# Kernel optimization log

Hardware: AMD Instinct MI355X
Metric: run time of the kernel (lower is better)

## Reference

```python
import jax, jax.numpy as jnp
import numpy as np

HIDDEN = 1024
NUM_HEADS = 8
HEAD_DIM = HIDDEN // NUM_HEADS
ROPE_BASE = 10000.0
RMS_EPS = 1e-6


def _rotate_half(x):
    # interleaved rotate: (x0,x1,x2,x3,...) -> (-x1,x0,-x3,x2,...)
    x1 = x[..., ::2]
    x2 = x[..., 1::2]
    return jnp.stack([-x2, x1], axis=-1).reshape(x.shape)


def _rope_cos_sin(seq_len, rotary_dim, dtype):
    inv_freq = 1.0 / (ROPE_BASE ** (jnp.arange(0, rotary_dim, 2, dtype=jnp.float32) / rotary_dim))
    pos = jnp.arange(seq_len, dtype=jnp.float32)
    freqs = pos[:, None] * inv_freq[None, :]            # [S, rd/2]
    cos = jnp.repeat(jnp.cos(freqs), 2, axis=-1)        # [S, rd]
    sin = jnp.repeat(jnp.sin(freqs), 2, axis=-1)
    return cos.astype(dtype)[None, None], sin.astype(dtype)[None, None]


def setup_inputs() -> dict:
    key = jax.random.key(0)
    k = jax.random.split(key, 8)
    B, S, H = 2, 2048, HIDDEN
    hidden_states = jax.random.normal(k[0], (B, S, H), dtype=jnp.float32)
    attention_mask = jax.random.randint(k[1], (B, S, S), 0, 2) > 0
    rel_ts_bias = jax.random.normal(k[2], (B, S, S), dtype=jnp.float32)
    s1 = 1.0 / np.sqrt(H)
    W_qkvu = jax.random.normal(k[3], (H, H * 6), dtype=jnp.float32) * s1
    W_out = jax.random.normal(k[4], (H * 3, H), dtype=jnp.float32) * (1.0 / np.sqrt(H * 3))
    b_out = jnp.zeros((H,), dtype=jnp.float32)
    rms_weight = jnp.ones((H,), dtype=jnp.float32)
    return {"hidden_states": hidden_states, "attention_mask": attention_mask,
            "rel_ts_bias": rel_ts_bias, "W_qkvu": W_qkvu, "W_out": W_out,
            "b_out": b_out, "rms_weight": rms_weight}


def reference(hidden_states, attention_mask, rel_ts_bias, W_qkvu, W_out, b_out, rms_weight):
    B, S, H = hidden_states.shape
    nh, hd = NUM_HEADS, HEAD_DIM
    fused = jax.nn.silu(hidden_states @ W_qkvu)          # [B,S,6H]
    gated = fused[..., :3 * H]                            # [B,S,3H]
    v = fused[..., 3 * H:4 * H].reshape(B, S, nh, hd).transpose(0, 2, 1, 3)
    q = fused[..., 4 * H:5 * H].reshape(B, S, nh, hd).transpose(0, 2, 1, 3)
    kk = fused[..., 5 * H:].reshape(B, S, nh, hd).transpose(0, 2, 1, 3)

    cos, sin = _rope_cos_sin(S, hd, hidden_states.dtype)  # rotary_dim == head_dim
    q_rope = q * cos + _rotate_half(q) * sin
    k_rope = kk * cos + _rotate_half(kk) * sin

    inv_s = 1.0 / max(S, 1)
    qk = jax.nn.relu(jnp.einsum('bhnd,bhmd->bhnm', q, kk)) * inv_s
    qk_rope = jax.nn.relu(jnp.einsum('bhnd,bhmd->bhnm', q_rope, k_rope)) * inv_s

    mask = attention_mask[:, None]                        # [B,1,S,S]
    qk = jnp.where(mask, qk, 0.0)
    qk_rope = jnp.where(mask, qk_rope, 0.0)
    ts_bias = jnp.where(attention_mask, rel_ts_bias, 0.0)

    ts_out = jnp.einsum('bnm,bhmd->bnhd', ts_bias, v)
    rope_out = jnp.einsum('bhnm,bhmd->bnhd', qk_rope, v)
    plain_out = jnp.einsum('bhnm,bhmd->bnhd', qk, v)

    combined = jnp.concatenate([rope_out, ts_out, plain_out], axis=-1).reshape(B, S, 3 * H)
    out = (combined * gated) @ W_out + b_out
    y = out + hidden_states
    rms = jax.lax.rsqrt(jnp.mean(y * y, axis=-1, keepdims=True) + RMS_EPS)
    return y * rms * rms_weight
```

## Files before the change

kernel.cpp:

```cpp
#include <hip/hip_runtime.h>
#include <math.h>

static constexpr int Bz = 2;
static constexpr int Sq = 2048;
static constexpr int Hh = 1024;
static constexpr int NH = 8;
static constexpr int HD = 128;
static constexpr int H3 = 3072;
static constexpr int H6 = 6144;

typedef unsigned short ushort_t;
typedef float f32x4v __attribute__((ext_vector_type(4)));
typedef short s16x8 __attribute__((ext_vector_type(8)));

static constexpr size_t FUSED_OFF = 0;
static constexpr size_t A2_OFF    = 12582912;
static constexpr size_t HB_OFF    = 18874368;
static constexpr size_t WQT_OFF   = 20971520;
static constexpr size_t WOT_OFF   = 24117248;
static constexpr size_t QR_OFF    = 25690112;
static constexpr size_t KR_OFF    = 27787264;
static constexpr size_t VT_OFF    = 29884416;
static constexpr size_t TAB_OFF   = 31981568;
static constexpr size_t FLAG_OFF  = 32243712;
static constexpr size_t TSB_OFF   = 32243716;
static constexpr size_t MBITS_OFF = 36438020;

__device__ __forceinline__ float silu_(float x) { return x / (1.0f + expf(-x)); }
__device__ __forceinline__ ushort_t f2bf(float x) {
  unsigned int u = __float_as_uint(x);
  u += 0x7fffu + ((u >> 16) & 1u);
  return (ushort_t)(u >> 16);
}
__device__ __forceinline__ float bf2f(ushort_t u) {
  return __uint_as_float(((unsigned int)u) << 16);
}
__device__ __forceinline__ void g2l16(const ushort_t* g, ushort_t* l) {
  __builtin_amdgcn_global_load_lds(
      (const __attribute__((address_space(1))) unsigned int*)g,
      (__attribute__((address_space(3))) unsigned int*)l, 16, 0, 0);
}

__global__ __launch_bounds__(256) void hstu_cvt_all(const float* __restrict__ hidden,
                                                    ushort_t* __restrict__ hb,
                                                    const float* __restrict__ Wq,
                                                    ushort_t* __restrict__ wqt,
                                                    const float* __restrict__ Wo,
                                                    ushort_t* __restrict__ wot,
                                                    float* __restrict__ tab,
                                                    const unsigned int* __restrict__ m,
                                                    int* __restrict__ flag) {
  __shared__ float tbuf[32][33];
  const int blk = blockIdx.x;
  if (blk >= 13824) {
    __shared__ int s_any;
    if (threadIdx.x == 0) s_any = 0;
    __syncthreads();
    int any = 0;
    for (int i = threadIdx.x; i < 8192; i += 256)
      if (m[i] > 1u) any = 1;
    if (any) s_any = 1;
    __syncthreads();
    if (threadIdx.x == 0) *flag = s_any;
    return;
  }
  if (blk >= 13312) {
    int t = (blk - 13312) * 256 + threadIdx.x;
    int i = t & 63;
    int s = t >> 6;
    float inv = powf(10000.0f, -(float)i / 64.0f);
    float sn, cs;
    sincosf((float)s * inv, &sn, &cs);
    tab[2 * t + 0] = cs;
    tab[2 * t + 1] = sn;
    return;
  }
  if (blk < 4096) {
    const int idx = blk * 256 + threadIdx.x;
    float4 v = *(const float4*)&hidden[(size_t)idx * 4];
    ushort4 o;
    o.x = f2bf(v.x); o.y = f2bf(v.y); o.z = f2bf(v.z); o.w = f2bf(v.w);
    *(ushort4*)&hb[(size_t)idx * 4] = o;
    return;
  }
  const float* in;
  ushort_t* out;
  int K, N, n0, k0;
  if (blk < 4096 + 6144) {
    const int j = blk - 4096;
    in = Wq; out = wqt; K = 1024; N = 6144;
    n0 = (j % 192) * 32; k0 = (j / 192) * 32;
  } else {
    const int j = blk - 10240;
    in = Wo; out = wot; K = 3072; N = 1024;
    n0 = (j % 32) * 32; k0 = (j / 32) * 32;
  }
  const int c = threadIdx.x & 31, rr = threadIdx.x >> 5;
#pragma unroll
  for (int p = 0; p < 4; ++p)
    tbuf[rr + p * 8][c] = in[(size_t)(k0 + rr + p * 8) * N + n0 + c];
  __syncthreads();
#pragma unroll
  for (int p = 0; p < 4; ++p)
    out[(size_t)(n0 + rr + p * 8) * K + k0 + c] = f2bf(tbuf[c][rr + p * 8]);
}

__global__ __launch_bounds__(256) void hstu_gemm_silu_msk(
    const ushort_t* __restrict__ A, const ushort_t* __restrict__ Bt,
    ushort_t* __restrict__ C, const int* __restrict__ mask32,
    const unsigned char* __restrict__ mask8, const int* __restrict__ mflag,
    const float* __restrict__ bias, ushort_t* __restrict__ tsb,
    unsigned char* __restrict__ mbits) {
  __shared__ ushort_t As[128 * 64];
  __shared__ ushort_t Bs[128 * 64];
  const int blk = blockIdx.x;
  const int tid = threadIdx.x;
  if (blk >= 1536) {
    const size_t gt = (size_t)(blk - 1536) * 256 + tid;
    const size_t base = gt * 8;
    const int m_u8 = *mflag;
    int mk[8];
    if (m_u8) {
      uchar4 a = *(const uchar4*)&mask8[base];
      uchar4 b = *(const uchar4*)&mask8[base + 4];
      mk[0] = a.x; mk[1] = a.y; mk[2] = a.z; mk[3] = a.w;
      mk[4] = b.x; mk[5] = b.y; mk[6] = b.z; mk[7] = b.w;
    } else {
      int4 a = *(const int4*)&mask32[base];
      int4 b = *(const int4*)&mask32[base + 4];
      mk[0] = a.x; mk[1] = a.y; mk[2] = a.z; mk[3] = a.w;
      mk[4] = b.x; mk[5] = b.y; mk[6] = b.z; mk[7] = b.w;
    }
    float4 b0 = *(const float4*)&bias[base];
    float4 b1 = *(const float4*)&bias[base + 4];
    float bb[8] = {b0.x, b0.y, b0.z, b0.w, b1.x, b1.y, b1.z, b1.w};
    ushort_t ts[8];
    unsigned int byte = 0;
#pragma unroll
    for (int i = 0; i < 8; ++i) {
      ts[i] = f2bf(mk[i] ? bb[i] : 0.0f);
      byte |= (mk[i] ? 1u : 0u) << i;
    }
    *(s16x8*)&tsb[base] = *(s16x8*)ts;
    mbits[gt] = (unsigned char)byte;
    return;
  }
  constexpr int K = 1024, N = H6;
  const int lane = tid & 63, wid = tid >> 6;
  const int lo4 = lane & 15, hi2 = lane >> 4;
  const int wr = wid >> 1, wc = wid & 1;
  const int row0 = (blk / 48) * 128, col0 = (blk % 48) * 128;
  const int srow = lane >> 3, scol = (lane & 7) * 8;
  f32x4v acc[4][4];
#pragma unroll
  for (int i = 0; i < 4; ++i)
#pragma unroll
    for (int j = 0; j < 4; ++j) acc[i][j] = {0.f, 0.f, 0.f, 0.f};

  for (int k0 = 0; k0 < K; k0 += 64) {
    __syncthreads();
#pragma unroll
    for (int i = 0; i < 4; ++i) {
      const int rb = wid * 32 + i * 8;
      g2l16(&A[(size_t)(row0 + rb + srow) * K + k0 + scol], &As[rb * 64]);
      g2l16(&Bt[(size_t)(col0 + rb + srow) * K + k0 + scol], &Bs[rb * 64]);
    }
    __syncthreads();
#pragma unroll
    for (int kc = 0; kc < 2; ++kc) {
      s16x8 af[4], bfr[4];
#pragma unroll
      for (int mi = 0; mi < 4; ++mi)
        af[mi] = *(const s16x8*)&As[(wr * 64 + mi * 16 + lo4) * 64 + kc * 32 + hi2 * 8];
#pragma unroll
      for (int nj = 0; nj < 4; ++nj)
        bfr[nj] = *(const s16x8*)&Bs[(wc * 64 + nj * 16 + lo4) * 64 + kc * 32 + hi2 * 8];
#pragma unroll
      for (int mi = 0; mi < 4; ++mi)
#pragma unroll
        for (int nj = 0; nj < 4; ++nj)
          acc[mi][nj] = __builtin_amdgcn_mfma_f32_16x16x32_bf16(af[mi], bfr[nj], acc[mi][nj], 0, 0, 0);
    }
  }
#pragma unroll
  for (int mi = 0; mi < 4; ++mi)
#pragma unroll
    for (int nj = 0; nj < 4; ++nj)
#pragma unroll
      for (int r = 0; r < 4; ++r) {
        const int row = row0 + wr * 64 + mi * 16 + hi2 * 4 + r;
        const int col = col0 + wc * 64 + nj * 16 + lo4;
        C[(size_t)row * N + col] = f2bf(silu_(acc[mi][nj][r]));
      }
}

__global__ __launch_bounds__(256) void hstu_prep2(const ushort_t* __restrict__ fused,
                                                  const float2* __restrict__ tab,
                                                  ushort_t* __restrict__ qr,
                                                  ushort_t* __restrict__ kr,
                                                  ushort_t* __restrict__ vt) {
  __shared__ ushort_t tbuf[32][36];
  const int blk = blockIdx.x;
  if (blk < 2048) {
    const int idx = blk * 256 + threadIdx.x;
    const int row = idx >> 7;
    const int cg = (idx & 127) * 8;
    const int s = row & (Sq - 1);
    const float2* trow = &tab[(size_t)s * 64 + ((cg & 127) >> 1)];
    float2 t[4];
#pragma unroll
    for (int p = 0; p < 4; ++p) t[p] = trow[p];
    s16x8 q8 = *(const s16x8*)&fused[(size_t)row * H6 + 4 * Hh + cg];
    s16x8 k8 = *(const s16x8*)&fused[(size_t)row * H6 + 5 * Hh + cg];
    ushort_t qo[8], ko[8];
#pragma unroll
    for (int p = 0; p < 4; ++p) {
      float qx = bf2f((ushort_t)q8[2 * p]), qy = bf2f((ushort_t)q8[2 * p + 1]);
      float kx = bf2f((ushort_t)k8[2 * p]), ky = bf2f((ushort_t)k8[2 * p + 1]);
      qo[2 * p] = f2bf(qx * t[p].x - qy * t[p].y);
      qo[2 * p + 1] = f2bf(qy * t[p].x + qx * t[p].y);
      ko[2 * p] = f2bf(kx * t[p].x - ky * t[p].y);
      ko[2 * p + 1] = f2bf(ky * t[p].x + kx * t[p].y);
    }
    *(s16x8*)&qr[(size_t)row * Hh + cg] = *(s16x8*)qo;
    *(s16x8*)&kr[(size_t)row * Hh + cg] = *(s16x8*)ko;
    return;
  }
  const int j = blk - 2048;
  const int m0 = (j & 63) * 32, d0 = ((j >> 6) & 3) * 32, bh = j >> 8;
  const int b = bh >> 3, h = bh & 7;
  const int r = threadIdx.x >> 3, cg = (threadIdx.x & 7) * 4;
  *(ushort4*)&tbuf[r][cg] =
      *(const ushort4*)&fused[(size_t)(b * Sq + m0 + r) * H6 + 3 * Hh + h * HD + d0 + cg];
  __syncthreads();
  ushort4 o;
  o.x = tbuf[cg + 0][r]; o.y = tbuf[cg + 1][r]; o.z = tbuf[cg + 2][r]; o.w = tbuf[cg + 3][r];
  *(ushort4*)&vt[(size_t)(bh * HD + d0 + r) * Sq + m0 + cg] = o;
}

__global__ __launch_bounds__(256) void hstu_gemm_out(const ushort_t* __restrict__ A,
                                                     const ushort_t* __restrict__ Bt,
                                                     const float* __restrict__ bout,
                                                     const float* __restrict__ hidden,
                                                     float* __restrict__ C) {
  constexpr int K = H3, N = Hh;
  __shared__ ushort_t As[128 * 64];
  __shared__ ushort_t Bs[64 * 64];
  const int tid = threadIdx.x, lane = tid & 63, wid = tid >> 6;
  const int lo4 = lane & 15, hi2 = lane >> 4;
  const int wr = wid >> 1, wc = wid & 1;
  const int row0 = blockIdx.y * 128, col0 = blockIdx.x * 64;
  const int srow = lane >> 3, scol = (lane & 7) * 8;
  f32x4v acc[4][2];
#pragma unroll
  for (int i = 0; i < 4; ++i)
#pragma unroll
    for (int j = 0; j < 2; ++j) acc[i][j] = {0.f, 0.f, 0.f, 0.f};

  for (int k0 = 0; k0 < K; k0 += 64) {
    __syncthreads();
#pragma unroll
    for (int i = 0; i < 4; ++i) {
      const int rb = wid * 32 + i * 8;
      g2l16(&A[(size_t)(row0 + rb + srow) * K + k0 + scol], &As[rb * 64]);
    }
#pragma unroll
    for (int i = 0; i < 2; ++i) {
      const int rb = wid * 16 + i * 8;
      g2l16(&Bt[(size_t)(col0 + rb + srow) * K + k0 + scol], &Bs[rb * 64]);
    }
    __syncthreads();
#pragma unroll
    for (int kc = 0; kc < 2; ++kc) {
      s16x8 af[4], bfr[2];
#pragma unroll
      for (int mi = 0; mi < 4; ++mi)
        af[mi] = *(const s16x8*)&As[(wr * 64 + mi * 16 + lo4) * 64 + kc * 32 + hi2 * 8];
#pragma unroll
      for (int nj = 0; nj < 2; ++nj)
        bfr[nj] = *(const s16x8*)&Bs[(wc * 32 + nj * 16 + lo4) * 64 + kc * 32 + hi2 * 8];
#pragma unroll
      for (int mi = 0; mi < 4; ++mi)
#pragma unroll
        for (int nj = 0; nj < 2; ++nj)
          acc[mi][nj] = __builtin_amdgcn_mfma_f32_16x16x32_bf16(af[mi], bfr[nj], acc[mi][nj], 0, 0, 0);
    }
  }
#pragma unroll
  for (int mi = 0; mi < 4; ++mi)
#pragma unroll
    for (int nj = 0; nj < 2; ++nj)
#pragma unroll
      for (int r = 0; r < 4; ++r) {
        const int row = row0 + wr * 64 + mi * 16 + hi2 * 4 + r;
        const int col = col0 + wc * 32 + nj * 16 + lo4;
        C[(size_t)row * N + col] = acc[mi][nj][r] + bout[col] + hidden[(size_t)row * N + col];
      }
}

__global__ __launch_bounds__(512, 4) void hstu_attn(const ushort_t* __restrict__ fused,
                                                    const ushort_t* __restrict__ qr,
                                                    const ushort_t* __restrict__ kr,
                                                    const ushort_t* __restrict__ vt,
                                                    const ushort_t* __restrict__ tsb,
                                                    const unsigned int* __restrict__ mbits32,
                                                    ushort_t* __restrict__ a2) {
  __shared__ __align__(16) ushort_t Ks[32][136];
  __shared__ __align__(16) ushort_t KRs[32][136];
  __shared__ __align__(16) ushort_t Vt[128][40];
  __shared__ __align__(16) ushort_t Pl[3][64][40];
  __shared__ unsigned int Mt32[64];

  const int tid = threadIdx.x;
  const int lane = tid & 63;
  const int wid = tid >> 6;
  const int lo4 = lane & 15;
  const int hi2 = lane >> 4;
  const int h = blockIdx.x;
  const int n0 = blockIdx.y * 64;
  const int b = blockIdx.z;
  const float ivs = 1.0f / 2048.0f;
  constexpr int NT = Sq / 32;

  const int krow = tid >> 4, kcol = (tid & 15) * 8;
  const int vdd = tid >> 2, vmg = (tid & 3) * 8;
  const int trow = (tid & 255) >> 2, tmg = (tid & 3) * 8;
  const size_t kbase = (size_t)b * Sq * H6 + 5 * Hh + h * HD + kcol;
  const size_t krbase = (size_t)b * Sq * Hh + h * HD + kcol;
  const size_t vbase = (size_t)((b * NH + h) * HD + vdd) * Sq + vmg;
  const size_t tbase = (size_t)(b * Sq + n0 + trow) * Sq + tmg;
  const size_t mbase = (size_t)(b * Sq + n0 + lane) * 64;

  const int t_w = wid >> 2;
  const int rq = wid & 3;
  s16x8 qf[4];
  {
    const int row = tid >> 4;
    const int colg = (tid & 15) * 8;
#pragma unroll
    for (int half = 0; half < 2; ++half) {
      const size_t gr = (size_t)(b * Sq + n0 + half * 32 + row);
      *(s16x8*)&Ks[row][colg] = *(const s16x8*)&fused[gr * H6 + 4 * Hh + h * HD + colg];
      *(s16x8*)&KRs[row][colg] = *(const s16x8*)&qr[gr * Hh + h * HD + colg];
      __syncthreads();
      if ((rq >> 1) == half) {
        const int lrow = (rq & 1) * 16 + lo4;
        const ushort_t(*Qsrc)[136] = t_w ? KRs : Ks;
#pragma unroll
        for (int c = 0; c < 4; ++c)
          qf[c] = *(const s16x8*)&Qsrc[lrow][c * 32 + hi2 * 8];
      }
      __syncthreads();
    }
  }

  const f32x4v zero4 = {0.f, 0.f, 0.f, 0.f};
  f32x4v accO[3][2][2];
#pragma unroll
  for (int t = 0; t < 3; ++t)
#pragma unroll
    for (int rt = 0; rt < 2; ++rt)
#pragma unroll
      for (int ct = 0; ct < 2; ++ct) accO[t][rt][ct] = zero4;

  const int rh2 = wid >> 2;
  const int cq = wid & 3;

  s16x8 kreg, krreg, vreg, tsreg;
  unsigned int mreg;
#define LOADT(T)                                                            \
  {                                                                         \
    const size_t moff = (size_t)(T) * 32;                                   \
    kreg = *(const s16x8*)&fused[kbase + (moff + krow) * H6];               \
    krreg = *(const s16x8*)&kr[krbase + (moff + krow) * Hh];                \
    vreg = *(const s16x8*)&vt[vbase + moff];                                \
    if (wid < 4) tsreg = *(const s16x8*)&tsb[tbase + moff];                 \
    else if (wid == 4) mreg = mbits32[mbase + (T)];                         \
  }
#define WRITET()                                                            \
  {                                                                         \
    *(s16x8*)&Ks[krow][kcol] = kreg;                                        \
    *(s16x8*)&KRs[krow][kcol] = krreg;                                      \
    *(s16x8*)&Vt[vdd][vmg] = vreg;                                          \
    if (wid < 4) *(s16x8*)&Pl[2][trow][tmg] = tsreg;                        \
    else if (wid == 4) Mt32[lane] = mreg;                                   \
  }

  LOADT(0);
  WRITET();
  __syncthreads();

  for (int t = 0; t < NT; ++t) {
    if (t + 1 < NT) LOADT(t + 1);
    {
      const ushort_t(*Kmat)[136] = t_w ? KRs : Ks;
      const int n = rq * 16 + lo4;
      const unsigned int bits = Mt32[n];
#pragma unroll
      for (int mt2 = 0; mt2 < 2; ++mt2) {
        f32x4v a = zero4;
#pragma unroll
        for (int c = 0; c < 4; ++c) {
          s16x8 kf = *(const s16x8*)&Kmat[mt2 * 16 + lo4][c * 32 + hi2 * 8];
          a = __builtin_amdgcn_mfma_f32_16x16x32_bf16(kf, qf[c], a, 0, 0, 0);
        }
        const int mb = mt2 * 16 + hi2 * 4;
        ushort4 po;
        po.x = ((bits >> (mb + 0)) & 1u) ? f2bf(fmaxf(a[0], 0.f) * ivs) : (ushort_t)0;
        po.y = ((bits >> (mb + 1)) & 1u) ? f2bf(fmaxf(a[1], 0.f) * ivs) : (ushort_t)0;
        po.z = ((bits >> (mb + 2)) & 1u) ? f2bf(fmaxf(a[2], 0.f) * ivs) : (ushort_t)0;
        po.w = ((bits >> (mb + 3)) & 1u) ? f2bf(fmaxf(a[3], 0.f) * ivs) : (ushort_t)0;
        *(ushort4*)&Pl[t_w][n][mb] = po;
      }
    }
    __syncthreads();
    {
      s16x8 af[3][2];
#pragma unroll
      for (int ty = 0; ty < 3; ++ty)
#pragma unroll
        for (int rt = 0; rt < 2; ++rt)
          af[ty][rt] = *(const s16x8*)&Pl[ty][rh2 * 32 + rt * 16 + lo4][hi2 * 8];
      s16x8 bfv[2];
#pragma unroll
      for (int ct = 0; ct < 2; ++ct)
        bfv[ct] = *(const s16x8*)&Vt[cq * 32 + ct * 16 + lo4][hi2 * 8];
#pragma unroll
      for (int ty = 0; ty < 3; ++ty)
#pragma unroll
        for (int rt = 0; rt < 2; ++rt)
#pragma unroll
          for (int ct = 0; ct < 2; ++ct)
            accO[ty][rt][ct] =
                __builtin_amdgcn_mfma_f32_16x16x32_bf16(af[ty][rt], bfv[ct], accO[ty][rt][ct], 0, 0, 0);
    }
    __syncthreads();
    if (t + 1 < NT) WRITET();
    __syncthreads();
  }
#undef LOADT
#undef WRITET

  const int toff[3] = {256, 0, 128};
#pragma unroll
  for (int ty = 0; ty < 3; ++ty)
#pragma unroll
    for (int rt = 0; rt < 2; ++rt)
#pragma unroll
      for (int ct = 0; ct < 2; ++ct)
#pragma unroll
        for (int r = 0; r < 4; ++r) {
          const int n = n0 + rh2 * 32 + rt * 16 + hi2 * 4 + r;
          const int dd = cq * 32 + ct * 16 + lo4;
          const int col3 = h * 384 + toff[ty] + dd;
          const float g = bf2f(fused[(size_t)(b * Sq + n) * H6 + col3]);
          a2[(size_t)(b * Sq + n) * H3 + col3] = f2bf(accO[ty][rt][ct][r] * g);
        }
}

__global__ __launch_bounds__(256) void hstu_rms(float* __restrict__ y,
                                                const float* __restrict__ w) {
  __shared__ float red[4];
  const int row = blockIdx.x;
  const int tid = threadIdx.x;
  float4 v = *(float4*)&y[(size_t)row * Hh + tid * 4];
  float ss = v.x * v.x + v.y * v.y + v.z * v.z + v.w * v.w;
#pragma unroll
  for (int o = 32; o > 0; o >>= 1) ss += __shfl_down(ss, o);
  if ((tid & 63) == 0) red[tid >> 6] = ss;
  __syncthreads();
  const float tot = red[0] + red[1] + red[2] + red[3];
  const float r = 1.0f / sqrtf(tot / (float)Hh + 1e-6f);
  float4 wv = *(const float4*)&w[tid * 4];
  v.x *= r * wv.x;
  v.y *= r * wv.y;
  v.z *= r * wv.z;
  v.w *= r * wv.w;
  *(float4*)&y[(size_t)row * Hh + tid * 4] = v;
}

extern "C" void kernel_launch(void* const* d_in, const int* in_sizes, int n_in,
                              void* d_out, int out_size, void* d_ws, size_t ws_size,
                              hipStream_t stream) {
  const float* hidden = (const float*)d_in[0];
  const void* mask = d_in[1];
  const float* bias = (const float*)d_in[2];
  const float* Wqkvu = (const float*)d_in[3];
  const float* Wout = (const float*)d_in[4];
  const float* bout = (const float*)d_in[5];
  const float* rmsw = (const float*)d_in[6];
  float* out = (float*)d_out;
  float* ws = (float*)d_ws;

  ushort_t* fused = (ushort_t*)(ws + FUSED_OFF);
  ushort_t* a2 = (ushort_t*)(ws + A2_OFF);
  ushort_t* hb = (ushort_t*)(ws + HB_OFF);
  ushort_t* wqt = (ushort_t*)(ws + WQT_OFF);
  ushort_t* wot = (ushort_t*)(ws + WOT_OFF);
  ushort_t* qrb = (ushort_t*)(ws + QR_OFF);
  ushort_t* krb = (ushort_t*)(ws + KR_OFF);
  ushort_t* vtb = (ushort_t*)(ws + VT_OFF);
  float* tab = ws + TAB_OFF;
  int* mflag = (int*)(ws + FLAG_OFF);
  ushort_t* tsbp = (ushort_t*)(ws + TSB_OFF);
  unsigned char* mbits = (unsigned char*)(ws + MBITS_OFF);

  hstu_cvt_all<<<13825, 256, 0, stream>>>(hidden, hb, Wqkvu, wqt, Wout, wot, tab,
                                          (const unsigned int*)mask, mflag);
  hstu_gemm_silu_msk<<<1536 + 4096, 256, 0, stream>>>(
      hb, wqt, fused, (const int*)mask, (const unsigned char*)mask, mflag, bias, tsbp, mbits);
  hstu_prep2<<<6144, 256, 0, stream>>>(fused, (const float2*)tab, qrb, krb, vtb);
  hstu_attn<<<dim3(NH, Sq / 64, Bz), 512, 0, stream>>>(
      fused, qrb, krb, vtb, tsbp, (const unsigned int*)mbits, a2);
  hstu_gemm_out<<<dim3(Hh / 64, (Bz * Sq) / 128), 256, 0, stream>>>(a2, wot, bout, hidden, out);
  hstu_rms<<<Bz * Sq, 256, 0, stream>>>(out, rmsw);
}
```

Before: 307.0 us.

## Fuse RoPE and V-transpose prep into the QKVU GEMM epilogue

Removes the separate prep kernel by computing rotary-embedded q/k and the transposed V directly in the epilogue of the silu GEMM. Tiles in the V column range write only the transposed layout and skip the fused buffer. Tiles in the Q/K ranges pair adjacent lanes via a shuffle to apply the rotation. This saves a kernel launch and a re-read of the fused activations. In exchange the GEMM epilogue has more scattered stores and table loads.

```diff
diff --git a/kernel.cpp b/kernel.cpp
--- a/kernel.cpp
+++ b/kernel.cpp
@@ -110,7 +110,9 @@
     ushort_t* __restrict__ C, const int* __restrict__ mask32,
     const unsigned char* __restrict__ mask8, const int* __restrict__ mflag,
     const float* __restrict__ bias, ushort_t* __restrict__ tsb,
-    unsigned char* __restrict__ mbits) {
+    unsigned char* __restrict__ mbits, const float2* __restrict__ tab2,
+    ushort_t* __restrict__ qr, ushort_t* __restrict__ kr,
+    ushort_t* __restrict__ vt) {
   __shared__ ushort_t As[128 * 64];
   __shared__ ushort_t Bs[128 * 64];
   const int blk = blockIdx.x;
@@ -182,6 +184,28 @@
           acc[mi][nj] = __builtin_amdgcn_mfma_f32_16x16x32_bf16(af[mi], bfr[nj], acc[mi][nj], 0, 0, 0);
     }
   }
+  if (col0 >= 3 * Hh && col0 < 4 * Hh) {
+    const int hh = (col0 - 3 * Hh) >> 7;
+#pragma unroll
+    for (int mi = 0; mi < 4; ++mi)
+#pragma unroll
+      for (int nj = 0; nj < 4; ++nj) {
+        ushort4 o;
+        o.x = f2bf(silu_(acc[mi][nj][0]));
+        o.y = f2bf(silu_(acc[mi][nj][1]));
+        o.z = f2bf(silu_(acc[mi][nj][2]));
+        o.w = f2bf(silu_(acc[mi][nj][3]));
+        const int row = row0 + wr * 64 + mi * 16 + hi2 * 4;
+        const int bb2 = row >> 11, ms = row & 2047;
+        const int dd = wc * 64 + nj * 16 + lo4;
+        *(ushort4*)&vt[(size_t)((bb2 * NH + hh) * HD + dd) * Sq + ms] = o;
+      }
+    return;
+  }
+  const bool isq = (col0 >= 4 * Hh) && (col0 < 5 * Hh);
+  const bool isk = (col0 >= 5 * Hh);
+  ushort_t* rdst = isq ? qr : kr;
+  const int dbase = col0 - (isq ? 4 * Hh : 5 * Hh);
 #pragma unroll
   for (int mi = 0; mi < 4; ++mi)
 #pragma unroll
@@ -190,52 +214,17 @@
       for (int r = 0; r < 4; ++r) {
         const int row = row0 + wr * 64 + mi * 16 + hi2 * 4 + r;
         const int col = col0 + wc * 64 + nj * 16 + lo4;
-        C[(size_t)row * N + col] = f2bf(silu_(acc[mi][nj][r]));
+        const ushort_t cb = f2bf(silu_(acc[mi][nj][r]));
+        C[(size_t)row * N + col] = cb;
+        if (isq || isk) {
+          const float v = bf2f(cb);
+          const float p = __shfl_xor(v, 1);
+          const int dfull = dbase + wc * 64 + nj * 16 + lo4;
+          const float2 cs = tab2[(size_t)(row & 2047) * 64 + ((dfull & 127) >> 1)];
+          const float o = (lane & 1) ? (v * cs.x + p * cs.y) : (v * cs.x - p * cs.y);
+          rdst[(size_t)row * Hh + dfull] = f2bf(o);
+        }
       }
-}
-
-__global__ __launch_bounds__(256) void hstu_prep2(const ushort_t* __restrict__ fused,
-                                                  const float2* __restrict__ tab,
-                                                  ushort_t* __restrict__ qr,
-                                                  ushort_t* __restrict__ kr,
-                                                  ushort_t* __restrict__ vt) {
-  __shared__ ushort_t tbuf[32][36];
-  const int blk = blockIdx.x;
-  if (blk < 2048) {
-    const int idx = blk * 256 + threadIdx.x;
-    const int row = idx >> 7;
-    const int cg = (idx & 127) * 8;
-    const int s = row & (Sq - 1);
-    const float2* trow = &tab[(size_t)s * 64 + ((cg & 127) >> 1)];
-    float2 t[4];
-#pragma unroll
-    for (int p = 0; p < 4; ++p) t[p] = trow[p];
-    s16x8 q8 = *(const s16x8*)&fused[(size_t)row * H6 + 4 * Hh + cg];
-    s16x8 k8 = *(const s16x8*)&fused[(size_t)row * H6 + 5 * Hh + cg];
-    ushort_t qo[8], ko[8];
-#pragma unroll
-    for (int p = 0; p < 4; ++p) {
-      float qx = bf2f((ushort_t)q8[2 * p]), qy = bf2f((ushort_t)q8[2 * p + 1]);
-      float kx = bf2f((ushort_t)k8[2 * p]), ky = bf2f((ushort_t)k8[2 * p + 1]);
-      qo[2 * p] = f2bf(qx * t[p].x - qy * t[p].y);
-      qo[2 * p + 1] = f2bf(qy * t[p].x + qx * t[p].y);
-      ko[2 * p] = f2bf(kx * t[p].x - ky * t[p].y);
-      ko[2 * p + 1] = f2bf(ky * t[p].x + kx * t[p].y);
-    }
-    *(s16x8*)&qr[(size_t)row * Hh + cg] = *(s16x8*)qo;
-    *(s16x8*)&kr[(size_t)row * Hh + cg] = *(s16x8*)ko;
-    return;
-  }
-  const int j = blk - 2048;
-  const int m0 = (j & 63) * 32, d0 = ((j >> 6) & 3) * 32, bh = j >> 8;
-  const int b = bh >> 3, h = bh & 7;
-  const int r = threadIdx.x >> 3, cg = (threadIdx.x & 7) * 4;
-  *(ushort4*)&tbuf[r][cg] =
-      *(const ushort4*)&fused[(size_t)(b * Sq + m0 + r) * H6 + 3 * Hh + h * HD + d0 + cg];
-  __syncthreads();
-  ushort4 o;
-  o.x = tbuf[cg + 0][r]; o.y = tbuf[cg + 1][r]; o.z = tbuf[cg + 2][r]; o.w = tbuf[cg + 3][r];
-  *(ushort4*)&vt[(size_t)(bh * HD + d0 + r) * Sq + m0 + cg] = o;
 }
 
 __global__ __launch_bounds__(256) void hstu_gemm_out(const ushort_t* __restrict__ A,
@@ -508,8 +497,8 @@
   hstu_cvt_all<<<13825, 256, 0, stream>>>(hidden, hb, Wqkvu, wqt, Wout, wot, tab,
                                           (const unsigned int*)mask, mflag);
   hstu_gemm_silu_msk<<<1536 + 4096, 256, 0, stream>>>(
-      hb, wqt, fused, (const int*)mask, (const unsigned char*)mask, mflag, bias, tsbp, mbits);
-  hstu_prep2<<<6144, 256, 0, stream>>>(fused, (const float2*)tab, qrb, krb, vtb);
+      hb, wqt, fused, (const int*)mask, (const unsigned char*)mask, mflag, bias, tsbp, mbits,
+      (const float2*)tab, qrb, krb, vtb);
   hstu_attn<<<dim3(NH, Sq / 64, Bz), 512, 0, stream>>>(
       fused, qrb, krb, vtb, tsbp, (const unsigned int*)mbits, a2);
   hstu_gemm_out<<<dim3(Hh / 64, (Bz * Sq) / 128), 256, 0, stream>>>(a2, wot, bout, hidden, out);
```

Measured after the change: 326.0 us. 1.06x slower.
